# Kernel tuning notes

Measured on AMD Instinct MI355X. Metric: run time of the kernel, lower is better.

## Reference

```python
import jax, jax.numpy as jnp
import numpy as np
import math

D_MODEL = 512
N_HEADS = 8
D_K = D_MODEL // N_HEADS
N_SAMPLES = 16
BETA = 1.0
SCALE = 1.0 / math.sqrt(D_K)
PROPOSAL_TEMP = 0.5


def setup_inputs() -> dict:
    key = jax.random.key(0)
    ks = jax.random.split(key, 9)
    B, S = 2, 512
    x = jax.random.normal(ks[0], (B, S, D_MODEL), dtype=jnp.float32)
    init = lambda k: jax.random.normal(k, (D_MODEL, D_MODEL), dtype=jnp.float32) * 0.02
    return {
        "x": x,
        "Wq": init(ks[1]), "bq": jnp.zeros((D_MODEL,), jnp.float32),
        "Wk": init(ks[2]), "bk": jnp.zeros((D_MODEL,), jnp.float32),
        "Wv": init(ks[3]), "bv": jnp.zeros((D_MODEL,), jnp.float32),
        "Wo": init(ks[4]), "bo": jnp.zeros((D_MODEL,), jnp.float32),
    }


def _importance_sampled_weights(scores):
    # scores: [B,H,S,S]. Replicates the per-row Python loop, fully vectorized.
    B, H, Sq, Sk = scores.shape
    target = jax.nn.softmax(scores * BETA, axis=-1)            # [B,H,Sq,Sk]
    # optimal proposal: 0.5*target + 0.5*uniform
    prop = PROPOSAL_TEMP * target + (1.0 - PROPOSAL_TEMP) / Sk
    R = B * H * Sq
    tf = target.reshape(R, Sk)
    pf = prop.reshape(R, Sk)
    # tsu_backend.sample_binary_layer(log(p/(1-p))) == Bernoulli(p) sampling
    s = jax.random.bernoulli(jax.random.key(42), pf[:, None, :], (R, N_SAMPLES, Sk))
    # importance weight = prod(target[sel]) / (prod(prop[sel]) * prod(1-prop[~sel]))
    pt = jnp.prod(jnp.where(s, tf[:, None, :], 1.0), axis=-1)                 # [R,N]
    pp = jnp.prod(jnp.where(s, pf[:, None, :], 1.0 - pf[:, None, :]), axis=-1)
    valid = (s.sum(-1) > 0) & (pp > 0)
    w = jnp.where(valid, pt / jnp.maximum(pp, 1e-38), 0.0)
    ws = w.sum(-1, keepdims=True)
    w = jnp.where(ws > 0, w / jnp.maximum(ws, 1e-38), 1.0 / N_SAMPLES)        # [R,N]
    wa = jnp.einsum('rn,rnk->rk', w, s.astype(jnp.float32))                   # [R,Sk]
    was = wa.sum(-1, keepdims=True)
    wa = jnp.where(was > 0, wa / jnp.maximum(was, 1e-38), 1.0 / Sk)
    return wa.reshape(B, H, Sq, Sk)


def reference(x, Wq, bq, Wk, bk, Wv, bv, Wo, bo):
    B, S, Dm = x.shape
    proj = lambda W, b: (x @ W + b).reshape(B, S, N_HEADS, D_K).transpose(0, 2, 1, 3)
    Q = proj(Wq, bq)  # [B,H,S,dk]
    K = proj(Wk, bk)
    V = proj(Wv, bv)
    scores = jnp.einsum('bhqd,bhkd->bhqk', Q, K) * SCALE
    # torch builds weights via torch.tensor(...) which detaches => constant w.r.t. params
    attn = jax.lax.stop_gradient(_importance_sampled_weights(scores))
    out = jnp.einsum('bhqk,bhkd->bhqd', attn, V)
    out = out.transpose(0, 2, 1, 3).reshape(B, S, Dm)
    return out @ Wo + bo
```

## Files before the change

### kernel.cpp

```cpp
#include <hip/hip_runtime.h>
#include <cstdint>
#include <cstddef>


#if __has_builtin(__builtin_amdgcn_alignbit)
#define ROTL(x, r) __builtin_amdgcn_alignbit((x), (x), 32 - (r))
#else
#define ROTL(x, r) (((x) << (r)) | ((x) >> (32 - (r))))
#endif

__device__ __forceinline__ void tf4_fold(uint32_t ca, uint32_t cb, uint32_t cc,
                                         uint32_t cd, uint32_t &ra,
                                         uint32_t &rb, uint32_t &rc,
                                         uint32_t &rd) {
  uint32_t a0 = 0u, a1 = ca, b0 = 0u, b1 = cb;
  uint32_t c0 = 0u, c1 = cc, d0 = 0u, d1 = cd;
#define QR(s)                                                                 \
  a0 += a1; b0 += b1; c0 += c1; d0 += d1;                                     \
  a1 = ROTL(a1, s); b1 = ROTL(b1, s); c1 = ROTL(c1, s); d1 = ROTL(d1, s);     \
  a1 ^= a0; b1 ^= b0; c1 ^= c0; d1 ^= d0;
#define INJ(x, y)                                                             \
  a0 += (x); b0 += (x); c0 += (x); d0 += (x);                                 \
  a1 += (y); b1 += (y); c1 += (y); d1 += (y);
  QR(13) QR(15) QR(26) QR(6)
  INJ(42u, 0x1BD11BF1u)
  QR(17) QR(29) QR(16) QR(24)
  INJ(0x1BD11BF0u, 2u)
  QR(13) QR(15) QR(26) QR(6)
  a1 += 45u; b1 += 45u; c1 += 45u; d1 += 45u;
  QR(17) QR(29) QR(16) QR(24)
  INJ(42u, 0x1BD11BF4u)
  QR(13) QR(15) QR(26) QR(6)
  INJ(0x1BD11BF0u, 5u)
#undef QR
#undef INJ
  ra = a0 ^ a1; rb = b0 ^ b1; rc = c0 ^ c1; rd = d0 ^ d1;
}

__global__ __launch_bounds__(256)
void qkv_gemm(const float* __restrict__ x,
              const float* __restrict__ Wq, const float* __restrict__ bq,
              const float* __restrict__ Wk, const float* __restrict__ bk,
              const float* __restrict__ Wv, const float* __restrict__ bv,
              float* __restrict__ Qw, float* __restrict__ KTw,
              float* __restrict__ Vw) {
  const float* W; const float* bias; float* out;
  if (blockIdx.z == 0)      { W = Wq; bias = bq; out = Qw; }
  else if (blockIdx.z == 1) { W = Wk; bias = bk; out = KTw; }
  else                      { W = Wv; bias = bv; out = Vw; }

  __shared__ float At[32][68];
  __shared__ float Bs[32][64];
  const int tid = threadIdx.x;
  const int tx = tid & 15, ty = tid >> 4;
  const int row0 = blockIdx.x * 64, col0 = blockIdx.y * 64;
  float acc[4][4] = {};

  for (int kk = 0; kk < 512; kk += 32) {
    const int ar = tid >> 2;
#pragma unroll
    for (int i = 0; i < 2; ++i) {
      const int kc = ((tid & 3) << 3) + (i << 2);
      const float4 a4 =
          *(const float4*)&x[(size_t)(row0 + ar) * 512 + kk + kc];
      At[kc + 0][ar] = a4.x; At[kc + 1][ar] = a4.y;
      At[kc + 2][ar] = a4.z; At[kc + 3][ar] = a4.w;
    }
#pragma unroll
    for (int i = 0; i < 2; ++i) {
      const int idx = tid + (i << 8);
      const int br = idx >> 4, bc = (idx & 15) << 2;
      *(float4*)&Bs[br][bc] =
          *(const float4*)&W[(size_t)(kk + br) * 512 + col0 + bc];
    }
    __syncthreads();
#pragma unroll
    for (int p = 0; p < 32; ++p) {
      const float4 a4 = *(const float4*)&At[p][ty << 2];
      const float4 b4 = *(const float4*)&Bs[p][tx << 2];
      acc[0][0] = fmaf(a4.x, b4.x, acc[0][0]); acc[0][1] = fmaf(a4.x, b4.y, acc[0][1]);
      acc[0][2] = fmaf(a4.x, b4.z, acc[0][2]); acc[0][3] = fmaf(a4.x, b4.w, acc[0][3]);
      acc[1][0] = fmaf(a4.y, b4.x, acc[1][0]); acc[1][1] = fmaf(a4.y, b4.y, acc[1][1]);
      acc[1][2] = fmaf(a4.y, b4.z, acc[1][2]); acc[1][3] = fmaf(a4.y, b4.w, acc[1][3]);
      acc[2][0] = fmaf(a4.z, b4.x, acc[2][0]); acc[2][1] = fmaf(a4.z, b4.y, acc[2][1]);
      acc[2][2] = fmaf(a4.z, b4.z, acc[2][2]); acc[2][3] = fmaf(a4.z, b4.w, acc[2][3]);
      acc[3][0] = fmaf(a4.w, b4.x, acc[3][0]); acc[3][1] = fmaf(a4.w, b4.y, acc[3][1]);
      acc[3][2] = fmaf(a4.w, b4.z, acc[3][2]); acc[3][3] = fmaf(a4.w, b4.w, acc[3][3]);
    }
    __syncthreads();
  }
  const bool isK = (blockIdx.z == 1);
#pragma unroll
  for (int i = 0; i < 4; ++i) {
    const int row = row0 + (ty << 2) + i;
    const int b = row >> 9, s = row & 511;
#pragma unroll
    for (int j = 0; j < 4; ++j) {
      const int col = col0 + (tx << 2) + j;
      const int h = col >> 6, d = col & 63;
      const float v = acc[i][j] + bias[col];
      if (isK)
        out[(((size_t)(b * 8 + h) * 64 + d) * 512) + s] = v;
      else
        out[(((size_t)(b * 8 + h) * 512 + s) * 64) + d] = v;
    }
  }
}

__global__ __launch_bounds__(256)
void out_gemm(const float* __restrict__ A, const float* __restrict__ W,
              const float* __restrict__ bias, float* __restrict__ C) {
  __shared__ float At[32][68];
  __shared__ float Bs[32][64];
  const int tid = threadIdx.x;
  const int tx = tid & 15, ty = tid >> 4;
  const int row0 = blockIdx.x * 64, col0 = blockIdx.y * 64;
  float acc[4][4] = {};

  for (int kk = 0; kk < 512; kk += 32) {
    const int ar = tid >> 2;
#pragma unroll
    for (int i = 0; i < 2; ++i) {
      const int kc = ((tid & 3) << 3) + (i << 2);
      const float4 a4 =
          *(const float4*)&A[(size_t)(row0 + ar) * 512 + kk + kc];
      At[kc + 0][ar] = a4.x; At[kc + 1][ar] = a4.y;
      At[kc + 2][ar] = a4.z; At[kc + 3][ar] = a4.w;
    }
#pragma unroll
    for (int i = 0; i < 2; ++i) {
      const int idx = tid + (i << 8);
      const int br = idx >> 4, bc = (idx & 15) << 2;
      *(float4*)&Bs[br][bc] =
          *(const float4*)&W[(size_t)(kk + br) * 512 + col0 + bc];
    }
    __syncthreads();
#pragma unroll
    for (int p = 0; p < 32; ++p) {
      const float4 a4 = *(const float4*)&At[p][ty << 2];
      const float4 b4 = *(const float4*)&Bs[p][tx << 2];
      acc[0][0] = fmaf(a4.x, b4.x, acc[0][0]); acc[0][1] = fmaf(a4.x, b4.y, acc[0][1]);
      acc[0][2] = fmaf(a4.x, b4.z, acc[0][2]); acc[0][3] = fmaf(a4.x, b4.w, acc[0][3]);
      acc[1][0] = fmaf(a4.y, b4.x, acc[1][0]); acc[1][1] = fmaf(a4.y, b4.y, acc[1][1]);
      acc[1][2] = fmaf(a4.y, b4.z, acc[1][2]); acc[1][3] = fmaf(a4.y, b4.w, acc[1][3]);
      acc[2][0] = fmaf(a4.z, b4.x, acc[2][0]); acc[2][1] = fmaf(a4.z, b4.y, acc[2][1]);
      acc[2][2] = fmaf(a4.z, b4.z, acc[2][2]); acc[2][3] = fmaf(a4.z, b4.w, acc[2][3]);
      acc[3][0] = fmaf(a4.w, b4.x, acc[3][0]); acc[3][1] = fmaf(a4.w, b4.y, acc[3][1]);
      acc[3][2] = fmaf(a4.w, b4.z, acc[3][2]); acc[3][3] = fmaf(a4.w, b4.w, acc[3][3]);
    }
    __syncthreads();
  }
#pragma unroll
  for (int i = 0; i < 4; ++i) {
    const int row = row0 + (ty << 2) + i;
#pragma unroll
    for (int j = 0; j < 4; ++j) {
      const int col = col0 + (tx << 2) + j;
      C[(size_t)row * 512 + col] = acc[i][j] + bias[col];
    }
  }
}

__global__ __launch_bounds__(256)
void scores_softmax(const float* __restrict__ Q, const float* __restrict__ KT,
                    float* __restrict__ tf_g) {
  const int blk = blockIdx.x;
  const int bh = blk >> 7, q0 = (blk & 127) << 2;
  const int tid = threadIdx.x;
  __shared__ __align__(16) float qs[4][64];
  __shared__ float redm[4][4], reds[4][4];
  qs[tid >> 6][tid & 63] =
      Q[((size_t)bh * 512 + q0 + (tid >> 6)) * 64 + (tid & 63)];
  __syncthreads();

  float sc[4][2];
#pragma unroll
  for (int ii = 0; ii < 2; ++ii) {
    const int k = tid + ii * 256;
    const float* Kp = KT + (size_t)bh * 64 * 512 + k;
    float a0 = 0.f, a1 = 0.f, a2 = 0.f, a3 = 0.f;
#pragma unroll
    for (int d4 = 0; d4 < 16; ++d4) {
      const float4 v0 = ((const float4*)qs[0])[d4];
      const float4 v1 = ((const float4*)qs[1])[d4];
      const float4 v2 = ((const float4*)qs[2])[d4];
      const float4 v3 = ((const float4*)qs[3])[d4];
      const float k0 = Kp[(size_t)(d4 * 4 + 0) * 512];
      const float k1 = Kp[(size_t)(d4 * 4 + 1) * 512];
      const float k2 = Kp[(size_t)(d4 * 4 + 2) * 512];
      const float k3 = Kp[(size_t)(d4 * 4 + 3) * 512];
      a0 = fmaf(v0.x, k0, a0); a0 = fmaf(v0.y, k1, a0);
      a0 = fmaf(v0.z, k2, a0); a0 = fmaf(v0.w, k3, a0);
      a1 = fmaf(v1.x, k0, a1); a1 = fmaf(v1.y, k1, a1);
      a1 = fmaf(v1.z, k2, a1); a1 = fmaf(v1.w, k3, a1);
      a2 = fmaf(v2.x, k0, a2); a2 = fmaf(v2.y, k1, a2);
      a2 = fmaf(v2.z, k2, a2); a2 = fmaf(v2.w, k3, a2);
      a3 = fmaf(v3.x, k0, a3); a3 = fmaf(v3.y, k1, a3);
      a3 = fmaf(v3.z, k2, a3); a3 = fmaf(v3.w, k3, a3);
    }
    sc[0][ii] = a0 * 0.125f; sc[1][ii] = a1 * 0.125f;
    sc[2][ii] = a2 * 0.125f; sc[3][ii] = a3 * 0.125f;
  }
  float mx[4];
#pragma unroll
  for (int i = 0; i < 4; ++i) mx[i] = fmaxf(sc[i][0], sc[i][1]);
  for (int m = 1; m < 64; m <<= 1) {
#pragma unroll
    for (int i = 0; i < 4; ++i) mx[i] = fmaxf(mx[i], __shfl_xor(mx[i], m));
  }
  if ((tid & 63) == 0) {
    const int w = tid >> 6;
#pragma unroll
    for (int i = 0; i < 4; ++i) redm[i][w] = mx[i];
  }
  __syncthreads();
  float ex[4][2], sm[4];
#pragma unroll
  for (int i = 0; i < 4; ++i) {
    const float rm = fmaxf(fmaxf(redm[i][0], redm[i][1]),
                           fmaxf(redm[i][2], redm[i][3]));
    ex[i][0] = expf(sc[i][0] - rm);
    ex[i][1] = expf(sc[i][1] - rm);
    sm[i] = ex[i][0] + ex[i][1];
  }
  for (int m = 1; m < 64; m <<= 1) {
#pragma unroll
    for (int i = 0; i < 4; ++i) sm[i] += __shfl_xor(sm[i], m);
  }
  if ((tid & 63) == 0) {
    const int w = tid >> 6;
#pragma unroll
    for (int i = 0; i < 4; ++i) reds[i][w] = sm[i];
  }
  __syncthreads();
#pragma unroll
  for (int i = 0; i < 4; ++i) {
    const float tot = reds[i][0] + reds[i][1] + reds[i][2] + reds[i][3];
    tf_g[((size_t)bh * 512 + q0 + i) * 512 + tid]       = ex[i][0] / tot;
    tf_g[((size_t)bh * 512 + q0 + i) * 512 + tid + 256] = ex[i][1] / tot;
  }
}

__global__ __launch_bounds__(256)
void sample_attnv(const float* __restrict__ tf_g, const float* __restrict__ V,
                  float* __restrict__ ao) {
  const int r = blockIdx.x;
  const int b = r >> 12, h = (r >> 9) & 7, q = r & 511;
  const int tid = threadIdx.x;
  __shared__ float tf[512];
  __shared__ __align__(16) uint32_t pscu[512];
  __shared__ float wa[512];
  __shared__ float wr[16];
  __shared__ float redc[8];
  __shared__ float psum[4][64];
  __shared__ int   list[512];
  __shared__ int   cnt;

  if (tid == 0) cnt = 0;
  {
    const float t0 = tf_g[(size_t)r * 512 + tid];
    const float t1 = tf_g[(size_t)r * 512 + tid + 256];
    tf[tid] = t0; tf[tid + 256] = t1;
    wa[tid] = 0.f; wa[tid + 256] = 0.f;
    const float p0 = fmaf(0.5f, t0, 0.0009765625f);
    const float p1 = fmaf(0.5f, t1, 0.0009765625f);
    pscu[tid]       = ((uint32_t)ceilf(p0 * 8388608.0f)) << 9;
    pscu[tid + 256] = ((uint32_t)ceilf(p1 * 8388608.0f)) << 9;
    float ql = (1.f - p0) * (1.f - p1);
    for (int m = 1; m < 64; m <<= 1) ql *= __shfl_xor(ql, m);
    if ((tid & 63) == 0) redc[4 + (tid >> 6)] = ql;
  }
  __syncthreads();
  const float Qrow = redc[4] * redc[5] * redc[6] * redc[7];

  const int n = tid >> 4, t = tid & 15;
  const int k0 = t << 5;
  uint4 pvv[8];
#pragma unroll
  for (int j = 0; j < 8; ++j) pvv[j] = *(const uint4*)&pscu[k0 + (j << 2)];

  const uint32_t cbase =
      (uint32_t)r * 8192u + (uint32_t)n * 512u + (uint32_t)k0 + 42u;
  uint32_t bits = 0u;
#pragma unroll
  for (int j = 0; j < 32; j += 4) {
    uint32_t ra, rb, rc, rd;
    tf4_fold(cbase + (uint32_t)j, cbase + (uint32_t)j + 1u,
             cbase + (uint32_t)j + 2u, cbase + (uint32_t)j + 3u,
             ra, rb, rc, rd);
    const uint4 p4 = pvv[j >> 2];
    bits |= (ra < p4.x ? 1u : 0u) << j;
    bits |= (rb < p4.y ? 1u : 0u) << (j + 1);
    bits |= (rc < p4.z ? 1u : 0u) << (j + 2);
    bits |= (rd < p4.w ? 1u : 0u) << (j + 3);
  }

  float ptl = 1.f, ratl = 1.f;
  int cl = __popc(bits);
  {
    uint32_t bb = bits;
    while (bb) {
      const int j = __builtin_ctz(bb);
      bb &= bb - 1u;
      const float tv = tf[k0 + j];
      const float p = fmaf(0.5f, tv, 0.0009765625f);
      ptl *= tv;
      ratl *= p / (1.f - p);
    }
  }
#pragma unroll
  for (int m = 1; m < 16; m <<= 1) {
    ptl *= __shfl_xor(ptl, m);
    ratl *= __shfl_xor(ratl, m);
    cl += __shfl_xor(cl, m);
  }
  if (t == 0) {
    const float pp = Qrow * ratl;
    wr[n] = (cl > 0 && pp > 0.f) ? (ptl / fmaxf(pp, 1e-38f)) : 0.f;
  }
  __syncthreads();
  float wsum = 0.f;
#pragma unroll
  for (int m2 = 0; m2 < 16; ++m2) wsum += wr[m2];
  const float wn = (wsum > 0.f) ? (wr[n] / fmaxf(wsum, 1e-38f)) : 0.0625f;
  {
    uint32_t bb = bits;
    while (bb) {
      const int j = __builtin_ctz(bb);
      bb &= bb - 1u;
      atomicAdd(&wa[k0 + j], wn);
    }
  }
  __syncthreads();

  float sp = wa[tid] + wa[tid + 256];
  for (int m = 1; m < 64; m <<= 1) sp += __shfl_xor(sp, m);
  if ((tid & 63) == 0) redc[tid >> 6] = sp;
  if (wa[tid] > 0.f)       { const int i = atomicAdd(&cnt, 1); list[i] = tid; }
  if (wa[tid + 256] > 0.f) { const int i = atomicAdd(&cnt, 1); list[i] = tid + 256; }
  __syncthreads();
  const float was = redc[0] + redc[1] + redc[2] + redc[3];
  const int nnz = cnt;

  const int g = tid >> 6, d = tid & 63;
  const float* Vb = V + ((size_t)(b * 8 + h) * 512) * 64;
  float acc = 0.f;
  if (was > 0.f) {
    const float inv = 1.f / fmaxf(was, 1e-38f);
    for (int i = g; i < nnz; i += 4) {
      const int k = list[i];
      acc = fmaf(wa[k] * inv, Vb[(size_t)k * 64 + d], acc);
    }
  } else {
    for (int k = g; k < 512; k += 4) acc += Vb[(size_t)k * 64 + d];
    acc *= 0.001953125f;
  }
  psum[g][d] = acc;
  __syncthreads();
  if (g == 0) {
    ao[((size_t)(b * 512 + q) * 512) + h * 64 + d] =
        psum[0][d] + psum[1][d] + psum[2][d] + psum[3][d];
  }
}

extern "C" void kernel_launch(void* const* d_in, const int* in_sizes, int n_in,
                              void* d_out, int out_size, void* d_ws,
                              size_t ws_size, hipStream_t stream) {
  const float* x  = (const float*)d_in[0];
  const float* Wq = (const float*)d_in[1];
  const float* bq = (const float*)d_in[2];
  const float* Wk = (const float*)d_in[3];
  const float* bk = (const float*)d_in[4];
  const float* Wv = (const float*)d_in[5];
  const float* bv = (const float*)d_in[6];
  const float* Wo = (const float*)d_in[7];
  const float* bo = (const float*)d_in[8];
  float* out = (float*)d_out;

  float* ws = (float*)d_ws;
  float* Qw = ws;
  float* KT = ws + 524288;
  float* Vw = ws + 1048576;
  float* tf = ws + 1572864;
  float* ao = ws + 5767168;

  dim3 gq(16, 8, 3);
  qkv_gemm<<<gq, 256, 0, stream>>>(x, Wq, bq, Wk, bk, Wv, bv, Qw, KT, Vw);
  scores_softmax<<<2048, 256, 0, stream>>>(Qw, KT, tf);
  sample_attnv<<<8192, 256, 0, stream>>>(tf, Vw, ao);
  dim3 go(16, 8);
  out_gemm<<<go, 256, 0, stream>>>(ao, Wo, bo, out);
}
```

Before: 273.1 us.

## Stage K tiles in LDS for scores and swizzle sampler threshold layout

The scores kernel now copies 16-row chunks of K^T into shared memory with float4 loads and reads them from LDS, instead of issuing strided scalar global loads per thread. The sampler stores the Bernoulli thresholds in a transposed shared layout so each 16-thread group reads contiguous uint4 values without bank conflicts, and loads them on demand rather than keeping 32 values in registers. Threefry is computed eight lanes at a time for more instruction-level parallelism. The trade-offs are an extra 32KB of LDS per block in the scores kernel, which may lower occupancy, plus added barriers and higher register pressure from the eight-wide hash state.

```diff
diff --git a/kernel.cpp b/kernel.cpp
--- a/kernel.cpp
+++ b/kernel.cpp
@@ -9,33 +9,22 @@
 #define ROTL(x, r) (((x) << (r)) | ((x) >> (32 - (r))))
 #endif
 
-__device__ __forceinline__ void tf4_fold(uint32_t ca, uint32_t cb, uint32_t cc,
-                                         uint32_t cd, uint32_t &ra,
-                                         uint32_t &rb, uint32_t &rc,
-                                         uint32_t &rd) {
-  uint32_t a0 = 0u, a1 = ca, b0 = 0u, b1 = cb;
-  uint32_t c0 = 0u, c1 = cc, d0 = 0u, d1 = cd;
-#define QR(s)                                                                 \
-  a0 += a1; b0 += b1; c0 += c1; d0 += d1;                                     \
-  a1 = ROTL(a1, s); b1 = ROTL(b1, s); c1 = ROTL(c1, s); d1 = ROTL(d1, s);     \
-  a1 ^= a0; b1 ^= b0; c1 ^= c0; d1 ^= d0;
-#define INJ(x, y)                                                             \
-  a0 += (x); b0 += (x); c0 += (x); d0 += (x);                                 \
-  a1 += (y); b1 += (y); c1 += (y); d1 += (y);
-  QR(13) QR(15) QR(26) QR(6)
-  INJ(42u, 0x1BD11BF1u)
-  QR(17) QR(29) QR(16) QR(24)
-  INJ(0x1BD11BF0u, 2u)
-  QR(13) QR(15) QR(26) QR(6)
-  a1 += 45u; b1 += 45u; c1 += 45u; d1 += 45u;
-  QR(17) QR(29) QR(16) QR(24)
-  INJ(42u, 0x1BD11BF4u)
-  QR(13) QR(15) QR(26) QR(6)
-  INJ(0x1BD11BF0u, 5u)
-#undef QR
-#undef INJ
-  ra = a0 ^ a1; rb = b0 ^ b1; rc = c0 ^ c1; rd = d0 ^ d1;
-}
+#define QR8(s)                                                                \
+  x0[0]+=x1[0];x0[1]+=x1[1];x0[2]+=x1[2];x0[3]+=x1[3];                        \
+  x0[4]+=x1[4];x0[5]+=x1[5];x0[6]+=x1[6];x0[7]+=x1[7];                        \
+  x1[0]=ROTL(x1[0],s);x1[1]=ROTL(x1[1],s);x1[2]=ROTL(x1[2],s);                \
+  x1[3]=ROTL(x1[3],s);x1[4]=ROTL(x1[4],s);x1[5]=ROTL(x1[5],s);                \
+  x1[6]=ROTL(x1[6],s);x1[7]=ROTL(x1[7],s);                                    \
+  x1[0]^=x0[0];x1[1]^=x0[1];x1[2]^=x0[2];x1[3]^=x0[3];                        \
+  x1[4]^=x0[4];x1[5]^=x0[5];x1[6]^=x0[6];x1[7]^=x0[7];
+#define INJ8(X, Y)                                                            \
+  x0[0]+=(X);x0[1]+=(X);x0[2]+=(X);x0[3]+=(X);                                \
+  x0[4]+=(X);x0[5]+=(X);x0[6]+=(X);x0[7]+=(X);                                \
+  x1[0]+=(Y);x1[1]+=(Y);x1[2]+=(Y);x1[3]+=(Y);                                \
+  x1[4]+=(Y);x1[5]+=(Y);x1[6]+=(Y);x1[7]+=(Y);
+#define INJ8Y(Y)                                                              \
+  x1[0]+=(Y);x1[1]+=(Y);x1[2]+=(Y);x1[3]+=(Y);                                \
+  x1[4]+=(Y);x1[5]+=(Y);x1[6]+=(Y);x1[7]+=(Y);
 
 __global__ __launch_bounds__(256)
 void qkv_gemm(const float* __restrict__ x,
@@ -168,38 +157,52 @@
   const int bh = blk >> 7, q0 = (blk & 127) << 2;
   const int tid = threadIdx.x;
   __shared__ __align__(16) float qs[4][64];
+  __shared__ __align__(16) float Ks[16][512];
   __shared__ float redm[4][4], reds[4][4];
   qs[tid >> 6][tid & 63] =
       Q[((size_t)bh * 512 + q0 + (tid >> 6)) * 64 + (tid & 63)];
-  __syncthreads();
-
+
+  float a[4][2] = {};
+  const float* KTb = KT + (size_t)bh * 64 * 512;
+  for (int c = 0; c < 4; ++c) {
+    __syncthreads();
+#pragma unroll
+    for (int i = 0; i < 8; ++i) {
+      const int slot = tid + (i << 8);
+      const int dr = slot >> 7, dc = (slot & 127) << 2;
+      *(float4*)&Ks[dr][dc] =
+          *(const float4*)&KTb[(size_t)(c * 16 + dr) * 512 + dc];
+    }
+    __syncthreads();
+#pragma unroll
+    for (int ii = 0; ii < 2; ++ii) {
+      const int k = tid + (ii << 8);
+#pragma unroll
+      for (int d4 = 0; d4 < 4; ++d4) {
+        const float k0 = Ks[d4 * 4 + 0][k];
+        const float k1 = Ks[d4 * 4 + 1][k];
+        const float k2 = Ks[d4 * 4 + 2][k];
+        const float k3 = Ks[d4 * 4 + 3][k];
+        const float4 v0 = ((const float4*)qs[0])[c * 4 + d4];
+        const float4 v1 = ((const float4*)qs[1])[c * 4 + d4];
+        const float4 v2 = ((const float4*)qs[2])[c * 4 + d4];
+        const float4 v3 = ((const float4*)qs[3])[c * 4 + d4];
+        a[0][ii] = fmaf(v0.x, k0, a[0][ii]); a[0][ii] = fmaf(v0.y, k1, a[0][ii]);
+        a[0][ii] = fmaf(v0.z, k2, a[0][ii]); a[0][ii] = fmaf(v0.w, k3, a[0][ii]);
+        a[1][ii] = fmaf(v1.x, k0, a[1][ii]); a[1][ii] = fmaf(v1.y, k1, a[1][ii]);
+        a[1][ii] = fmaf(v1.z, k2, a[1][ii]); a[1][ii] = fmaf(v1.w, k3, a[1][ii]);
+        a[2][ii] = fmaf(v2.x, k0, a[2][ii]); a[2][ii] = fmaf(v2.y, k1, a[2][ii]);
+        a[2][ii] = fmaf(v2.z, k2, a[2][ii]); a[2][ii] = fmaf(v2.w, k3, a[2][ii]);
+        a[3][ii] = fmaf(v3.x, k0, a[3][ii]); a[3][ii] = fmaf(v3.y, k1, a[3][ii]);
+        a[3][ii] = fmaf(v3.z, k2, a[3][ii]); a[3][ii] = fmaf(v3.w, k3, a[3][ii]);
+      }
+    }
+  }
   float sc[4][2];
 #pragma unroll
-  for (int ii = 0; ii < 2; ++ii) {
-    const int k = tid + ii * 256;
-    const float* Kp = KT + (size_t)bh * 64 * 512 + k;
-    float a0 = 0.f, a1 = 0.f, a2 = 0.f, a3 = 0.f;
-#pragma unroll
-    for (int d4 = 0; d4 < 16; ++d4) {
-      const float4 v0 = ((const float4*)qs[0])[d4];
-      const float4 v1 = ((const float4*)qs[1])[d4];
-      const float4 v2 = ((const float4*)qs[2])[d4];
-      const float4 v3 = ((const float4*)qs[3])[d4];
-      const float k0 = Kp[(size_t)(d4 * 4 + 0) * 512];
-      const float k1 = Kp[(size_t)(d4 * 4 + 1) * 512];
-      const float k2 = Kp[(size_t)(d4 * 4 + 2) * 512];
-      const float k3 = Kp[(size_t)(d4 * 4 + 3) * 512];
-      a0 = fmaf(v0.x, k0, a0); a0 = fmaf(v0.y, k1, a0);
-      a0 = fmaf(v0.z, k2, a0); a0 = fmaf(v0.w, k3, a0);
-      a1 = fmaf(v1.x, k0, a1); a1 = fmaf(v1.y, k1, a1);
-      a1 = fmaf(v1.z, k2, a1); a1 = fmaf(v1.w, k3, a1);
-      a2 = fmaf(v2.x, k0, a2); a2 = fmaf(v2.y, k1, a2);
-      a2 = fmaf(v2.z, k2, a2); a2 = fmaf(v2.w, k3, a2);
-      a3 = fmaf(v3.x, k0, a3); a3 = fmaf(v3.y, k1, a3);
-      a3 = fmaf(v3.z, k2, a3); a3 = fmaf(v3.w, k3, a3);
-    }
-    sc[0][ii] = a0 * 0.125f; sc[1][ii] = a1 * 0.125f;
-    sc[2][ii] = a2 * 0.125f; sc[3][ii] = a3 * 0.125f;
+  for (int i = 0; i < 4; ++i) {
+    sc[i][0] = a[i][0] * 0.125f;
+    sc[i][1] = a[i][1] * 0.125f;
   }
   float mx[4];
 #pragma unroll
@@ -248,7 +251,7 @@
   const int b = r >> 12, h = (r >> 9) & 7, q = r & 511;
   const int tid = threadIdx.x;
   __shared__ float tf[512];
-  __shared__ __align__(16) uint32_t pscu[512];
+  __shared__ __align__(16) uint32_t pscu2[512];
   __shared__ float wa[512];
   __shared__ float wr[16];
   __shared__ float redc[8];
@@ -264,8 +267,16 @@
     wa[tid] = 0.f; wa[tid + 256] = 0.f;
     const float p0 = fmaf(0.5f, t0, 0.0009765625f);
     const float p1 = fmaf(0.5f, t1, 0.0009765625f);
-    pscu[tid]       = ((uint32_t)ceilf(p0 * 8388608.0f)) << 9;
-    pscu[tid + 256] = ((uint32_t)ceilf(p1 * 8388608.0f)) << 9;
+    {
+      const int k = tid;
+      pscu2[(((k & 31) >> 2) << 6) + ((k >> 5) << 2) + (k & 3)] =
+          ((uint32_t)ceilf(p0 * 8388608.0f)) << 9;
+    }
+    {
+      const int k = tid + 256;
+      pscu2[(((k & 31) >> 2) << 6) + ((k >> 5) << 2) + (k & 3)] =
+          ((uint32_t)ceilf(p1 * 8388608.0f)) << 9;
+    }
     float ql = (1.f - p0) * (1.f - p1);
     for (int m = 1; m < 64; m <<= 1) ql *= __shfl_xor(ql, m);
     if ((tid & 63) == 0) redc[4 + (tid >> 6)] = ql;
@@ -275,24 +286,34 @@
 
   const int n = tid >> 4, t = tid & 15;
   const int k0 = t << 5;
-  uint4 pvv[8];
-#pragma unroll
-  for (int j = 0; j < 8; ++j) pvv[j] = *(const uint4*)&pscu[k0 + (j << 2)];
-
   const uint32_t cbase =
       (uint32_t)r * 8192u + (uint32_t)n * 512u + (uint32_t)k0 + 42u;
   uint32_t bits = 0u;
 #pragma unroll
-  for (int j = 0; j < 32; j += 4) {
-    uint32_t ra, rb, rc, rd;
-    tf4_fold(cbase + (uint32_t)j, cbase + (uint32_t)j + 1u,
-             cbase + (uint32_t)j + 2u, cbase + (uint32_t)j + 3u,
-             ra, rb, rc, rd);
-    const uint4 p4 = pvv[j >> 2];
-    bits |= (ra < p4.x ? 1u : 0u) << j;
-    bits |= (rb < p4.y ? 1u : 0u) << (j + 1);
-    bits |= (rc < p4.z ? 1u : 0u) << (j + 2);
-    bits |= (rd < p4.w ? 1u : 0u) << (j + 3);
+  for (int jb = 0; jb < 32; jb += 8) {
+    uint32_t x0[8], x1[8];
+#pragma unroll
+    for (int i = 0; i < 8; ++i) { x0[i] = 0u; x1[i] = cbase + (uint32_t)(jb + i); }
+    QR8(13) QR8(15) QR8(26) QR8(6)
+    INJ8(42u, 0x1BD11BF1u)
+    QR8(17) QR8(29) QR8(16) QR8(24)
+    INJ8(0x1BD11BF0u, 2u)
+    QR8(13) QR8(15) QR8(26) QR8(6)
+    INJ8Y(45u)
+    QR8(17) QR8(29) QR8(16) QR8(24)
+    INJ8(42u, 0x1BD11BF4u)
+    QR8(13) QR8(15) QR8(26) QR8(6)
+    INJ8(0x1BD11BF0u, 5u)
+    const uint4 pA = *(const uint4*)&pscu2[((jb >> 2) << 6) + (t << 2)];
+    const uint4 pB = *(const uint4*)&pscu2[(((jb >> 2) + 1) << 6) + (t << 2)];
+    bits |= (uint32_t)((x0[0] ^ x1[0]) < pA.x) << (jb + 0);
+    bits |= (uint32_t)((x0[1] ^ x1[1]) < pA.y) << (jb + 1);
+    bits |= (uint32_t)((x0[2] ^ x1[2]) < pA.z) << (jb + 2);
+    bits |= (uint32_t)((x0[3] ^ x1[3]) < pA.w) << (jb + 3);
+    bits |= (uint32_t)((x0[4] ^ x1[4]) < pB.x) << (jb + 4);
+    bits |= (uint32_t)((x0[5] ^ x1[5]) < pB.y) << (jb + 5);
+    bits |= (uint32_t)((x0[6] ^ x1[6]) < pB.z) << (jb + 6);
+    bits |= (uint32_t)((x0[7] ^ x1[7]) < pB.w) << (jb + 7);
   }
 
   float ptl = 1.f, ratl = 1.f;
```

Measured after the change: 284.9 us. 1.04x slower.
